# Kernel tuning notes

Hardware: AMD Instinct MI355X
Metric: run time of the kernel (lower is better)

The kernel has to match this reference:

```python
import jax, jax.numpy as jnp
import numpy as np

B, S, D, A, O = 4, 4096, 256, 64, 256

def setup_inputs() -> dict:
    key = jax.random.key(0)
    k1, k2, k3, k4, k5 = jax.random.split(key, 5)
    x = jax.random.normal(k1, (B, S, D), dtype=jnp.float32)
    # weights stored as [in, out] so projection is x @ W (same math as torch Linear W^T)
    Wk = jax.random.normal(k2, (D, A), dtype=jnp.float32) * (1.0 / np.sqrt(D))
    Wq = jax.random.normal(k3, (D, A), dtype=jnp.float32) * (1.0 / np.sqrt(D))
    Wv = jax.random.normal(k4, (D, A), dtype=jnp.float32) * (1.0 / np.sqrt(D))
    Wo = jax.random.normal(k5, (A, O), dtype=jnp.float32) * (1.0 / np.sqrt(A))
    return {"x": x, "Wk": Wk, "Wq": Wq, "Wv": Wv, "Wo": Wo}

def reference(x, Wk, Wq, Wv, Wo):
    # Single-head self-attention; dropout is identity at inference.
    k = x @ Wk  # [B,S,A]
    q = x @ Wq  # [B,S,A]
    v = x @ Wv  # [B,S,A]
    scale = 1.0 / jnp.sqrt(jnp.asarray(A, x.dtype))
    # logits[b,s,t] = k[b,s,:] . q[b,t,:]   (K @ Q^T in the torch code)
    logits = jnp.einsum('bsa,bta->bst', k, q) * scale
    w = jax.nn.softmax(logits, axis=-1)  # softmax over t
    # out[b,s,:] = sum_t w[b,s,t] * v[b,t,:]  (equivalent to V @ w^T then transpose)
    attn = jnp.einsum('bst,bta->bsa', w, v)
    return attn @ Wo  # [B,S,O]
```

## Files before the change

### kernel.cpp

```cpp
#include <hip/hip_runtime.h>


#define SQN 4096
#define AN 64
#define ON 256
#define QP 72

typedef short bf16x8 __attribute__((ext_vector_type(8)));
typedef float f32x4 __attribute__((ext_vector_type(4)));

__device__ __forceinline__ unsigned short f2bf(float f) {
    unsigned int u = __float_as_uint(f);
    u += 0x7fffu + ((u >> 16) & 1u);
    return (unsigned short)(u >> 16);
}
__device__ __forceinline__ unsigned int pack2(float a, float b) {
    return (unsigned int)f2bf(a) | ((unsigned int)f2bf(b) << 16);
}
__device__ __forceinline__ float exp2_hw(float x) {
    float r; asm("v_exp_f32 %0, %1" : "=v"(r) : "v"(x)); return r;
}

__global__ __launch_bounds__(256) void k_wtrans(
    const float* __restrict__ Wk, const float* __restrict__ Wq,
    const float* __restrict__ Wv, const float* __restrict__ Wo,
    unsigned short* __restrict__ WT, unsigned short* __restrict__ WoT)
{
    int bidx = blockIdx.x, tid = threadIdx.x;
    if (bidx < 24) {
        int m = bidx >> 3, chunk = bidx & 7;
        const float* src = (m == 0) ? Wk : (m == 1) ? Wq : Wv;
        float scl = (m == 1) ? 0.18033688011112042f : 1.0f;
        unsigned short* dst = WT + (m * 64 + chunk * 8) * 256;
        for (int idx = tid; idx < 8 * 256; idx += 256) {
            int a = chunk * 8 + (idx >> 8), d = idx & 255;
            dst[idx] = f2bf(src[d * 64 + a] * scl);
        }
    } else {
        int chunk = bidx - 24;
        for (int idx = tid; idx < 32 * 64; idx += 256) {
            int o = chunk * 32 + (idx >> 6), a = idx & 63;
            WoT[o * 64 + a] = f2bf(Wo[a * 256 + o]);
        }
    }
}

__global__ __launch_bounds__(256) void k_proj(
    const float* __restrict__ x, const unsigned short* __restrict__ WT,
    unsigned short* __restrict__ Ko, unsigned short* __restrict__ Qo,
    unsigned short* __restrict__ VTo)
{
    __shared__ unsigned short w_lds[192 * 128];
    __shared__ unsigned short x_lds[64 * 128];
    const int tid = threadIdx.x;
    const int wid = tid >> 6, lane = tid & 63, g = lane >> 4, li = lane & 15;
    const int s0 = blockIdx.x * 64;

    f32x4 acc[3][4] = {};
    for (int dh = 0; dh < 2; ++dh) {
        __syncthreads();
        {
            int row = tid >> 2, seg = tid & 3;
            const float4* src = (const float4*)(x + (size_t)(s0 + row) * 256 + dh * 128 + seg * 32);
            #pragma unroll
            for (int c = 0; c < 4; ++c) {
                float4 v0 = src[2 * c], v1 = src[2 * c + 1];
                uint4 o;
                o.x = pack2(v0.x, v0.y); o.y = pack2(v0.z, v0.w);
                o.z = pack2(v1.x, v1.y); o.w = pack2(v1.z, v1.w);
                *(uint4*)((char*)x_lds + row * 256 + ((seg * 64 + c * 16) ^ ((row & 7) << 4))) = o;
            }
        }
        {
            #pragma unroll
            for (int c = 0; c < 12; ++c) {
                int ch = tid + 256 * c;
                int row = ch >> 4, k16 = ch & 15;
                uint4 v = *(const uint4*)(WT + row * 256 + dh * 128 + k16 * 8);
                *(uint4*)((char*)w_lds + row * 256 + ((k16 * 16) ^ ((row & 7) << 4))) = v;
            }
        }
        __syncthreads();
        #pragma unroll
        for (int dc = 0; dc < 4; ++dc) {
            bf16x8 afr[4];
            #pragma unroll
            for (int sf = 0; sf < 4; ++sf) {
                int ar = sf * 16 + li;
                afr[sf] = *(const bf16x8*)((char*)x_lds + ar * 256 + ((dc * 64 + 16 * g) ^ ((ar & 7) << 4)));
            }
            #pragma unroll
            for (int c = 0; c < 3; ++c) {
                int br = (wid * 3 + c) * 16 + li;
                bf16x8 bfr = *(const bf16x8*)((char*)w_lds + br * 256 + ((dc * 64 + 16 * g) ^ ((br & 7) << 4)));
                #pragma unroll
                for (int sf = 0; sf < 4; ++sf)
                    acc[c][sf] = __builtin_amdgcn_mfma_f32_16x16x32_bf16(afr[sf], bfr, acc[c][sf], 0, 0, 0);
            }
        }
    }
    const int b = s0 >> 12;
    #pragma unroll
    for (int c = 0; c < 3; ++c) {
        int cfg = wid * 3 + c;
        int p = cfg >> 2, col = (cfg & 3) * 16 + li;
        if (p == 2) {
            int a = col;
            #pragma unroll
            for (int sf = 0; sf < 4; ++sf) {
                int sb = (s0 & 4095) + sf * 16 + 4 * g;
                uint2 u;
                u.x = pack2(acc[c][sf][0], acc[c][sf][1]);
                u.y = pack2(acc[c][sf][2], acc[c][sf][3]);
                *(uint2*)&VTo[(((size_t)(b * 64 + a)) << 12) + sb] = u;
            }
        } else {
            unsigned short* dst = (p == 0) ? Ko : Qo;
            #pragma unroll
            for (int sf = 0; sf < 4; ++sf)
                #pragma unroll
                for (int r = 0; r < 4; ++r)
                    dst[(size_t)(s0 + sf * 16 + 4 * g + r) * 64 + col] = f2bf(acc[c][sf][r]);
        }
    }
}

__global__ __launch_bounds__(256) void k_attn(
    const unsigned short* __restrict__ Qg, const unsigned short* __restrict__ Kg,
    const unsigned short* __restrict__ VTg,
    float* __restrict__ Opart, float* __restrict__ Mb, float* __restrict__ Lb)
{
    __shared__ unsigned short q_lds[2][64 * QP];
    __shared__ unsigned short v_lds[2][64 * QP];
    const int tid = threadIdx.x;
    const int wid = tid >> 6, lane = tid & 63, g = lane >> 4, li = lane & 15;
    const int b = blockIdx.x >> 8;
    const int s0 = ((blockIdx.x >> 2) & 63) * 64;
    const int h = blockIdx.x & 3;
    const int t_beg = h * 1024;
    const size_t base = (size_t)b * SQN * AN;
    const int srow = tid >> 2, sseg = tid & 3;

    bf16x8 kfrag[2];
    {
        const unsigned short* kp = Kg + base + (size_t)(s0 + wid * 16 + li) * 64;
        kfrag[0] = *(const bf16x8*)(kp + 8 * g);
        kfrag[1] = *(const bf16x8*)(kp + 32 + 8 * g);
    }

    {
        const uint4* qs = (const uint4*)(Qg + base + (size_t)(t_beg + srow) * 64 + sseg * 16);
        const uint4* vs = (const uint4*)(VTg + (((size_t)(b * 64 + srow)) << 12) + t_beg + sseg * 16);
        uint4 q0 = qs[0], q1 = qs[1], v0 = vs[0], v1 = vs[1];
        uint4* qd = (uint4*)&q_lds[0][srow * QP + sseg * 16];
        uint4* vd = (uint4*)&v_lds[0][srow * QP + sseg * 16];
        qd[0] = q0; qd[1] = q1; vd[0] = v0; vd[1] = v1;
    }
    __syncthreads();

    f32x4 ot[4] = {};
    float m_run = -1e30f, l_run = 0.0f;
    int cur = 0;

    for (int ti = 0; ti < 16; ++ti) {
        uint4 qr0, qr1, vr0, vr1;
        const bool pf = (ti < 15);
        if (pf) {
            int t1 = t_beg + (ti + 1) * 64;
            const uint4* qs = (const uint4*)(Qg + base + (size_t)(t1 + srow) * 64 + sseg * 16);
            const uint4* vs = (const uint4*)(VTg + (((size_t)(b * 64 + srow)) << 12) + t1 + sseg * 16);
            qr0 = qs[0]; qr1 = qs[1]; vr0 = vs[0]; vr1 = vs[1];
        }

        f32x4 st[4];
        #pragma unroll
        for (int tf = 0; tf < 4; ++tf) {
            f32x4 a0 = {};
            bf16x8 qa0 = *(const bf16x8*)&q_lds[cur][(tf * 16 + li) * QP + 8 * g];
            bf16x8 qa1 = *(const bf16x8*)&q_lds[cur][(tf * 16 + li) * QP + 32 + 8 * g];
            a0 = __builtin_amdgcn_mfma_f32_16x16x32_bf16(qa0, kfrag[0], a0, 0, 0, 0);
            a0 = __builtin_amdgcn_mfma_f32_16x16x32_bf16(qa1, kfrag[1], a0, 0, 0, 0);
            st[tf] = a0;
        }

        float tm = -1e30f;
        #pragma unroll
        for (int tf = 0; tf < 4; ++tf)
            #pragma unroll
            for (int r = 0; r < 4; ++r) tm = fmaxf(tm, st[tf][r]);
        tm = fmaxf(tm, __shfl_xor(tm, 16));
        tm = fmaxf(tm, __shfl_xor(tm, 32));
        float m_new = fmaxf(m_run, tm);
        float alpha = exp2_hw(m_run - m_new);
        float ts = 0.0f;
        unsigned int pk[4][2];
        #pragma unroll
        for (int tf = 0; tf < 4; ++tf) {
            float p0 = exp2_hw(st[tf][0] - m_new);
            float p1 = exp2_hw(st[tf][1] - m_new);
            float p2 = exp2_hw(st[tf][2] - m_new);
            float p3 = exp2_hw(st[tf][3] - m_new);
            ts += (p0 + p1) + (p2 + p3);
            pk[tf][0] = pack2(p0, p1);
            pk[tf][1] = pack2(p2, p3);
        }
        ts += __shfl_xor(ts, 16);
        ts += __shfl_xor(ts, 32);
        l_run = l_run * alpha + ts;
        m_run = m_new;
        #pragma unroll
        for (int af = 0; af < 4; ++af)
            #pragma unroll
            for (int r = 0; r < 4; ++r) ot[af][r] *= alpha;

        #pragma unroll
        for (int kc = 0; kc < 2; ++kc) {
            int s1 = ((2 * g) & 3) * 16 + li;
            int s2 = ((2 * g + 1) & 3) * 16 + li;
            unsigned int w0a = (unsigned)__shfl((int)pk[2 * kc][0], s1);
            unsigned int w1a = (unsigned)__shfl((int)pk[2 * kc][1], s1);
            unsigned int w2a = (unsigned)__shfl((int)pk[2 * kc][0], s2);
            unsigned int w3a = (unsigned)__shfl((int)pk[2 * kc][1], s2);
            unsigned int w0b = (unsigned)__shfl((int)pk[2 * kc + 1][0], s1);
            unsigned int w1b = (unsigned)__shfl((int)pk[2 * kc + 1][1], s1);
            unsigned int w2b = (unsigned)__shfl((int)pk[2 * kc + 1][0], s2);
            unsigned int w3b = (unsigned)__shfl((int)pk[2 * kc + 1][1], s2);
            union { unsigned int w[4]; bf16x8 v; } pb;
            bool hi = (g >= 2);
            pb.w[0] = hi ? w0b : w0a;
            pb.w[1] = hi ? w1b : w1a;
            pb.w[2] = hi ? w2b : w2a;
            pb.w[3] = hi ? w3b : w3a;
            #pragma unroll
            for (int af = 0; af < 4; ++af) {
                bf16x8 va = *(const bf16x8*)&v_lds[cur][(af * 16 + li) * QP + kc * 32 + 8 * g];
                ot[af] = __builtin_amdgcn_mfma_f32_16x16x32_bf16(va, pb.v, ot[af], 0, 0, 0);
            }
        }

        __syncthreads();
        if (pf) {
            uint4* qd = (uint4*)&q_lds[cur ^ 1][srow * QP + sseg * 16];
            uint4* vd = (uint4*)&v_lds[cur ^ 1][srow * QP + sseg * 16];
            qd[0] = qr0; qd[1] = qr1; vd[0] = vr0; vd[1] = vr1;
        }
        __syncthreads();
        cur ^= 1;
    }

    const int s = s0 + wid * 16 + li;
    float* op = Opart + ((size_t)((h * 4 + b) * 4096 + s)) * 64;
    #pragma unroll
    for (int af = 0; af < 4; ++af) {
        float4 o;
        o.x = ot[af][0]; o.y = ot[af][1]; o.z = ot[af][2]; o.w = ot[af][3];
        *(float4*)(op + af * 16 + 4 * g) = o;
    }
    if (g == 0) {
        Mb[(h * 4 + b) * 4096 + s] = m_run;
        Lb[(h * 4 + b) * 4096 + s] = l_run;
    }
}

__global__ __launch_bounds__(256) void k_combine_oproj(
    const float* __restrict__ Opart, const float* __restrict__ Mb, const float* __restrict__ Lb,
    const unsigned short* __restrict__ WoT, float* __restrict__ out)
{
    __shared__ unsigned short a_lds[64 * QP];
    const int tid = threadIdx.x;
    const int b = blockIdx.x >> 6;
    const int s0 = (blockIdx.x & 63) * 64;

    {
        int row = tid >> 2, seg = tid & 3;
        size_t ridx = (size_t)b * 4096 + s0 + row;
        float mm[4], ll[4];
        #pragma unroll
        for (int hh = 0; hh < 4; ++hh) { mm[hh] = Mb[hh * 16384 + ridx]; ll[hh] = Lb[hh * 16384 + ridx]; }
        float M = fmaxf(fmaxf(mm[0], mm[1]), fmaxf(mm[2], mm[3]));
        float w[4], denom = 0.0f;
        #pragma unroll
        for (int hh = 0; hh < 4; ++hh) { w[hh] = exp2_hw(mm[hh] - M); denom += w[hh] * ll[hh]; }
        float inv = 1.0f / denom;
        float av[16];
        #pragma unroll
        for (int j = 0; j < 16; ++j) av[j] = 0.0f;
        #pragma unroll
        for (int hh = 0; hh < 4; ++hh) {
            const float* op = Opart + ((size_t)hh * 16384 + ridx) * 64 + seg * 16;
            #pragma unroll
            for (int c = 0; c < 4; ++c) {
                float4 v = *(const float4*)(op + c * 4);
                av[4 * c + 0] += w[hh] * v.x; av[4 * c + 1] += w[hh] * v.y;
                av[4 * c + 2] += w[hh] * v.z; av[4 * c + 3] += w[hh] * v.w;
            }
        }
        uint4 u0, u1;
        u0.x = pack2(av[0] * inv, av[1] * inv);  u0.y = pack2(av[2] * inv, av[3] * inv);
        u0.z = pack2(av[4] * inv, av[5] * inv);  u0.w = pack2(av[6] * inv, av[7] * inv);
        u1.x = pack2(av[8] * inv, av[9] * inv);  u1.y = pack2(av[10] * inv, av[11] * inv);
        u1.z = pack2(av[12] * inv, av[13] * inv); u1.w = pack2(av[14] * inv, av[15] * inv);
        *(uint4*)&a_lds[row * QP + seg * 16] = u0;
        *(uint4*)&a_lds[row * QP + seg * 16 + 8] = u1;
    }
    __syncthreads();

    const int wid = tid >> 6, lane = tid & 63, g = lane >> 4, li = lane & 15;
    bf16x8 wf[4][2];
    #pragma unroll
    for (int of = 0; of < 4; ++of) {
        const unsigned short* wp = WoT + (size_t)(wid * 64 + of * 16 + li) * 64;
        wf[of][0] = *(const bf16x8*)(wp + 8 * g);
        wf[of][1] = *(const bf16x8*)(wp + 32 + 8 * g);
    }
    #pragma unroll
    for (int sf = 0; sf < 4; ++sf) {
        bf16x8 b0 = *(const bf16x8*)&a_lds[(sf * 16 + li) * QP + 8 * g];
        bf16x8 b1 = *(const bf16x8*)&a_lds[(sf * 16 + li) * QP + 32 + 8 * g];
        #pragma unroll
        for (int of = 0; of < 4; ++of) {
            f32x4 acc = {};
            acc = __builtin_amdgcn_mfma_f32_16x16x32_bf16(wf[of][0], b0, acc, 0, 0, 0);
            acc = __builtin_amdgcn_mfma_f32_16x16x32_bf16(wf[of][1], b1, acc, 0, 0, 0);
            float4 o;
            o.x = acc[0]; o.y = acc[1]; o.z = acc[2]; o.w = acc[3];
            *(float4*)&out[((size_t)b * 4096 + s0 + sf * 16 + li) * 256 + wid * 64 + of * 16 + 4 * g] = o;
        }
    }
}

extern "C" void kernel_launch(void* const* d_in, const int* in_sizes, int n_in,
                              void* d_out, int out_size, void* d_ws, size_t ws_size,
                              hipStream_t stream) {
    const float* x  = (const float*)d_in[0];
    const float* Wk = (const float*)d_in[1];
    const float* Wq = (const float*)d_in[2];
    const float* Wv = (const float*)d_in[3];
    const float* Wo = (const float*)d_in[4];
    float* out = (float*)d_out;

    char* ws = (char*)d_ws;
    unsigned short* WT  = (unsigned short*)(ws);
    unsigned short* WoT = (unsigned short*)(ws + 98304);
    unsigned short* Qb  = (unsigned short*)(ws + 131072);
    unsigned short* Kb  = (unsigned short*)(ws + 131072 + (1u<<21));
    unsigned short* VTb = (unsigned short*)(ws + 131072 + (2u<<21));
    float* Opart = (float*)(ws + 131072 + (3u<<21));
    float* Mb    = (float*)(ws + 131072 + (3u<<21) + (16u<<20));
    float* Lb    = (float*)(ws + 131072 + (3u<<21) + (17u<<20));

    k_wtrans<<<32, 256, 0, stream>>>(Wk, Wq, Wv, Wo, WT, WoT);
    k_proj<<<256, 256, 0, stream>>>(x, WT, Kb, Qb, VTb);
    k_attn<<<1024, 256, 0, stream>>>(Qb, Kb, VTb, Opart, Mb, Lb);
    k_combine_oproj<<<256, 256, 0, stream>>>(Opart, Mb, Lb, WoT, out);
}
```

Measured before the change: 135.0 us.

## Rework projection, attention and combine kernels with swizzled LDS and lazy rescaling

The projection kernel now handles 32 rows per block, reads weights directly from global memory instead of staging them in LDS, and launches twice as many blocks. The attention kernel swaps padded LDS rows for XOR-swizzled layouts, passes P through LDS instead of lane shuffles, and rescales the running max only when it grows past a threshold of 8. The combine kernel uses 16-row blocks to get more parallelism, and the bf16 conversion uses the hardware pack instruction. Together these aim to cut LDS bank conflicts, shuffle overhead and rescale work, but add more LDS traffic for P and rely on the threshold keeping exp values within range.

```diff
diff --git a/kernel.cpp b/kernel.cpp
--- a/kernel.cpp
+++ b/kernel.cpp
@@ -4,7 +4,6 @@
 #define SQN 4096
 #define AN 64
 #define ON 256
-#define QP 72
 
 typedef short bf16x8 __attribute__((ext_vector_type(8)));
 typedef float f32x4 __attribute__((ext_vector_type(4)));
@@ -14,8 +13,10 @@
     u += 0x7fffu + ((u >> 16) & 1u);
     return (unsigned short)(u >> 16);
 }
-__device__ __forceinline__ unsigned int pack2(float a, float b) {
-    return (unsigned int)f2bf(a) | ((unsigned int)f2bf(b) << 16);
+__device__ __forceinline__ unsigned int cvtpk(float lo, float hi) {
+    unsigned int r;
+    asm("v_cvt_pk_bf16_f32 %0, %1, %2" : "=v"(r) : "v"(lo), "v"(hi));
+    return r;
 }
 __device__ __forceinline__ float exp2_hw(float x) {
     float r; asm("v_exp_f32 %0, %1" : "=v"(r) : "v"(x)); return r;
@@ -50,74 +51,62 @@
     unsigned short* __restrict__ Ko, unsigned short* __restrict__ Qo,
     unsigned short* __restrict__ VTo)
 {
-    __shared__ unsigned short w_lds[192 * 128];
-    __shared__ unsigned short x_lds[64 * 128];
+    __shared__ unsigned short x_lds[32 * 256];
     const int tid = threadIdx.x;
     const int wid = tid >> 6, lane = tid & 63, g = lane >> 4, li = lane & 15;
-    const int s0 = blockIdx.x * 64;
-
-    f32x4 acc[3][4] = {};
-    for (int dh = 0; dh < 2; ++dh) {
-        __syncthreads();
-        {
-            int row = tid >> 2, seg = tid & 3;
-            const float4* src = (const float4*)(x + (size_t)(s0 + row) * 256 + dh * 128 + seg * 32);
-            #pragma unroll
-            for (int c = 0; c < 4; ++c) {
-                float4 v0 = src[2 * c], v1 = src[2 * c + 1];
-                uint4 o;
-                o.x = pack2(v0.x, v0.y); o.y = pack2(v0.z, v0.w);
-                o.z = pack2(v1.x, v1.y); o.w = pack2(v1.z, v1.w);
-                *(uint4*)((char*)x_lds + row * 256 + ((seg * 64 + c * 16) ^ ((row & 7) << 4))) = o;
-            }
-        }
-        {
-            #pragma unroll
-            for (int c = 0; c < 12; ++c) {
-                int ch = tid + 256 * c;
-                int row = ch >> 4, k16 = ch & 15;
-                uint4 v = *(const uint4*)(WT + row * 256 + dh * 128 + k16 * 8);
-                *(uint4*)((char*)w_lds + row * 256 + ((k16 * 16) ^ ((row & 7) << 4))) = v;
-            }
-        }
-        __syncthreads();
-        #pragma unroll
-        for (int dc = 0; dc < 4; ++dc) {
-            bf16x8 afr[4];
-            #pragma unroll
-            for (int sf = 0; sf < 4; ++sf) {
-                int ar = sf * 16 + li;
-                afr[sf] = *(const bf16x8*)((char*)x_lds + ar * 256 + ((dc * 64 + 16 * g) ^ ((ar & 7) << 4)));
-            }
-            #pragma unroll
-            for (int c = 0; c < 3; ++c) {
-                int br = (wid * 3 + c) * 16 + li;
-                bf16x8 bfr = *(const bf16x8*)((char*)w_lds + br * 256 + ((dc * 64 + 16 * g) ^ ((br & 7) << 4)));
-                #pragma unroll
-                for (int sf = 0; sf < 4; ++sf)
-                    acc[c][sf] = __builtin_amdgcn_mfma_f32_16x16x32_bf16(afr[sf], bfr, acc[c][sf], 0, 0, 0);
-            }
-        }
-    }
+    const int s0 = blockIdx.x * 32;
+
+    {
+        const float4* xs = (const float4*)(x + (size_t)s0 * 256);
+        #pragma unroll
+        for (int i = 0; i < 8; ++i) {
+            int idx4 = i * 256 + tid;
+            float4 v = xs[idx4];
+            int row = idx4 >> 6, q = idx4 & 63;
+            int unit = q >> 1, half = q & 1;
+            uint2 u; u.x = cvtpk(v.x, v.y); u.y = cvtpk(v.z, v.w);
+            *(uint2*)&x_lds[row * 256 + ((unit ^ (row & 7)) << 3) + half * 4] = u;
+        }
+    }
+    __syncthreads();
+
+    f32x4 acc[3][2] = {};
+    #pragma unroll
+    for (int dc = 0; dc < 8; ++dc) {
+        bf16x8 afr[2];
+        #pragma unroll
+        for (int sf = 0; sf < 2; ++sf) {
+            int ar = sf * 16 + li;
+            afr[sf] = *(const bf16x8*)&x_lds[ar * 256 + (((4 * dc + g) ^ (ar & 7)) << 3)];
+        }
+        #pragma unroll
+        for (int c = 0; c < 3; ++c) {
+            int wc = (wid * 3 + c) * 16 + li;
+            bf16x8 bfr = *(const bf16x8*)&WT[wc * 256 + dc * 32 + 8 * g];
+            #pragma unroll
+            for (int sf = 0; sf < 2; ++sf)
+                acc[c][sf] = __builtin_amdgcn_mfma_f32_16x16x32_bf16(afr[sf], bfr, acc[c][sf], 0, 0, 0);
+        }
+    }
+
     const int b = s0 >> 12;
     #pragma unroll
     for (int c = 0; c < 3; ++c) {
         int cfg = wid * 3 + c;
         int p = cfg >> 2, col = (cfg & 3) * 16 + li;
         if (p == 2) {
-            int a = col;
-            #pragma unroll
-            for (int sf = 0; sf < 4; ++sf) {
+            #pragma unroll
+            for (int sf = 0; sf < 2; ++sf) {
                 int sb = (s0 & 4095) + sf * 16 + 4 * g;
                 uint2 u;
-                u.x = pack2(acc[c][sf][0], acc[c][sf][1]);
-                u.y = pack2(acc[c][sf][2], acc[c][sf][3]);
-                *(uint2*)&VTo[(((size_t)(b * 64 + a)) << 12) + sb] = u;
+                u.x = cvtpk(acc[c][sf][0], acc[c][sf][1]);
+                u.y = cvtpk(acc[c][sf][2], acc[c][sf][3]);
+                *(uint2*)&VTo[(((size_t)(b * 64 + col)) << 12) + sb] = u;
             }
         } else {
             unsigned short* dst = (p == 0) ? Ko : Qo;
             #pragma unroll
-            for (int sf = 0; sf < 4; ++sf)
+            for (int sf = 0; sf < 2; ++sf)
                 #pragma unroll
                 for (int r = 0; r < 4; ++r)
                     dst[(size_t)(s0 + sf * 16 + 4 * g + r) * 64 + col] = f2bf(acc[c][sf][r]);
@@ -130,8 +119,9 @@
     const unsigned short* __restrict__ VTg,
     float* __restrict__ Opart, float* __restrict__ Mb, float* __restrict__ Lb)
 {
-    __shared__ unsigned short q_lds[2][64 * QP];
-    __shared__ unsigned short v_lds[2][64 * QP];
+    __shared__ unsigned short q_lds[2][64 * 64];
+    __shared__ unsigned short v_lds[2][64 * 64];
+    __shared__ unsigned int   p_lds[4][16 * 32];
     const int tid = threadIdx.x;
     const int wid = tid >> 6, lane = tid & 63, g = lane >> 4, li = lane & 15;
     const int b = blockIdx.x >> 8;
@@ -139,7 +129,8 @@
     const int h = blockIdx.x & 3;
     const int t_beg = h * 1024;
     const size_t base = (size_t)b * SQN * AN;
-    const int srow = tid >> 2, sseg = tid & 3;
+    const int srow = tid >> 2, sseg = tid & 3, r7 = srow & 7;
+    const int l7 = li & 7;
 
     bf16x8 kfrag[2];
     {
@@ -152,9 +143,10 @@
         const uint4* qs = (const uint4*)(Qg + base + (size_t)(t_beg + srow) * 64 + sseg * 16);
         const uint4* vs = (const uint4*)(VTg + (((size_t)(b * 64 + srow)) << 12) + t_beg + sseg * 16);
         uint4 q0 = qs[0], q1 = qs[1], v0 = vs[0], v1 = vs[1];
-        uint4* qd = (uint4*)&q_lds[0][srow * QP + sseg * 16];
-        uint4* vd = (uint4*)&v_lds[0][srow * QP + sseg * 16];
-        qd[0] = q0; qd[1] = q1; vd[0] = v0; vd[1] = v1;
+        *(uint4*)&q_lds[0][srow * 64 + (((2 * sseg) ^ r7) << 3)] = q0;
+        *(uint4*)&q_lds[0][srow * 64 + (((2 * sseg + 1) ^ r7) << 3)] = q1;
+        *(uint4*)&v_lds[0][srow * 64 + (((2 * sseg) ^ r7) << 3)] = v0;
+        *(uint4*)&v_lds[0][srow * 64 + (((2 * sseg + 1) ^ r7) << 3)] = v1;
     }
     __syncthreads();
 
@@ -176,8 +168,9 @@
         #pragma unroll
         for (int tf = 0; tf < 4; ++tf) {
             f32x4 a0 = {};
-            bf16x8 qa0 = *(const bf16x8*)&q_lds[cur][(tf * 16 + li) * QP + 8 * g];
-            bf16x8 qa1 = *(const bf16x8*)&q_lds[cur][(tf * 16 + li) * QP + 32 + 8 * g];
+            int qr = tf * 16 + li;
+            bf16x8 qa0 = *(const bf16x8*)&q_lds[cur][qr * 64 + ((g ^ l7) << 3)];
+            bf16x8 qa1 = *(const bf16x8*)&q_lds[cur][qr * 64 + (((4 + g) ^ l7) << 3)];
             a0 = __builtin_amdgcn_mfma_f32_16x16x32_bf16(qa0, kfrag[0], a0, 0, 0, 0);
             a0 = __builtin_amdgcn_mfma_f32_16x16x32_bf16(qa1, kfrag[1], a0, 0, 0, 0);
             st[tf] = a0;
@@ -190,59 +183,50 @@
             for (int r = 0; r < 4; ++r) tm = fmaxf(tm, st[tf][r]);
         tm = fmaxf(tm, __shfl_xor(tm, 16));
         tm = fmaxf(tm, __shfl_xor(tm, 32));
-        float m_new = fmaxf(m_run, tm);
-        float alpha = exp2_hw(m_run - m_new);
+        if (__any(tm > m_run + 8.0f)) {
+            float m_new = fmaxf(m_run, tm);
+            float alpha = exp2_hw(m_run - m_new);
+            #pragma unroll
+            for (int af = 0; af < 4; ++af)
+                #pragma unroll
+                for (int r = 0; r < 4; ++r) ot[af][r] *= alpha;
+            l_run *= alpha;
+            m_run = m_new;
+        }
         float ts = 0.0f;
-        unsigned int pk[4][2];
         #pragma unroll
         for (int tf = 0; tf < 4; ++tf) {
-            float p0 = exp2_hw(st[tf][0] - m_new);
-            float p1 = exp2_hw(st[tf][1] - m_new);
-            float p2 = exp2_hw(st[tf][2] - m_new);
-            float p3 = exp2_hw(st[tf][3] - m_new);
+            float p0 = exp2_hw(st[tf][0] - m_run);
+            float p1 = exp2_hw(st[tf][1] - m_run);
+            float p2 = exp2_hw(st[tf][2] - m_run);
+            float p3 = exp2_hw(st[tf][3] - m_run);
             ts += (p0 + p1) + (p2 + p3);
-            pk[tf][0] = pack2(p0, p1);
-            pk[tf][1] = pack2(p2, p3);
+            uint2 u; u.x = cvtpk(p0, p1); u.y = cvtpk(p2, p3);
+            int wi = 8 * tf + 2 * g;
+            *(uint2*)&p_lds[wid][li * 32 + (wi ^ (l7 << 2))] = u;
         }
         ts += __shfl_xor(ts, 16);
         ts += __shfl_xor(ts, 32);
-        l_run = l_run * alpha + ts;
-        m_run = m_new;
-        #pragma unroll
-        for (int af = 0; af < 4; ++af)
-            #pragma unroll
-            for (int r = 0; r < 4; ++r) ot[af][r] *= alpha;
+        l_run += ts;
 
         #pragma unroll
         for (int kc = 0; kc < 2; ++kc) {
-            int s1 = ((2 * g) & 3) * 16 + li;
-            int s2 = ((2 * g + 1) & 3) * 16 + li;
-            unsigned int w0a = (unsigned)__shfl((int)pk[2 * kc][0], s1);
-            unsigned int w1a = (unsigned)__shfl((int)pk[2 * kc][1], s1);
-            unsigned int w2a = (unsigned)__shfl((int)pk[2 * kc][0], s2);
-            unsigned int w3a = (unsigned)__shfl((int)pk[2 * kc][1], s2);
-            unsigned int w0b = (unsigned)__shfl((int)pk[2 * kc + 1][0], s1);
-            unsigned int w1b = (unsigned)__shfl((int)pk[2 * kc + 1][1], s1);
-            unsigned int w2b = (unsigned)__shfl((int)pk[2 * kc + 1][0], s2);
-            unsigned int w3b = (unsigned)__shfl((int)pk[2 * kc + 1][1], s2);
-            union { unsigned int w[4]; bf16x8 v; } pb;
-            bool hi = (g >= 2);
-            pb.w[0] = hi ? w0b : w0a;
-            pb.w[1] = hi ? w1b : w1a;
-            pb.w[2] = hi ? w2b : w2a;
-            pb.w[3] = hi ? w3b : w3a;
+            uint4 pw = *(const uint4*)&p_lds[wid][li * 32 + ((16 * kc + 4 * g) ^ (l7 << 2))];
+            union { uint4 u; bf16x8 v; } pb; pb.u = pw;
             #pragma unroll
             for (int af = 0; af < 4; ++af) {
-                bf16x8 va = *(const bf16x8*)&v_lds[cur][(af * 16 + li) * QP + kc * 32 + 8 * g];
+                int vr = af * 16 + li;
+                bf16x8 va = *(const bf16x8*)&v_lds[cur][vr * 64 + (((4 * kc + g) ^ (vr & 7)) << 3)];
                 ot[af] = __builtin_amdgcn_mfma_f32_16x16x32_bf16(va, pb.v, ot[af], 0, 0, 0);
             }
         }
 
         __syncthreads();
         if (pf) {
-            uint4* qd = (uint4*)&q_lds[cur ^ 1][srow * QP + sseg * 16];
-            uint4* vd = (uint4*)&v_lds[cur ^ 1][srow * QP + sseg * 16];
-            qd[0] = qr0; qd[1] = qr1; vd[0] = vr0; vd[1] = vr1;
+            *(uint4*)&q_lds[cur ^ 1][srow * 64 + (((2 * sseg) ^ r7) << 3)] = qr0;
+            *(uint4*)&q_lds[cur ^ 1][srow * 64 + (((2 * sseg + 1) ^ r7) << 3)] = qr1;
+            *(uint4*)&v_lds[cur ^ 1][srow * 64 + (((2 * sseg) ^ r7) << 3)] = vr0;
+            *(uint4*)&v_lds[cur ^ 1][srow * 64 + (((2 * sseg + 1) ^ r7) << 3)] = vr1;
         }
         __syncthreads();
         cur ^= 1;
@@ -266,13 +250,13 @@
     const float* __restrict__ Opart, const float* __restrict__ Mb, const float* __restrict__ Lb,
     const unsigned short* __restrict__ WoT, float* __restrict__ out)
 {
-    __shared__ unsigned short a_lds[64 * QP];
+    __shared__ unsigned short a_lds[16 * 64];
     const int tid = threadIdx.x;
-    const int b = blockIdx.x >> 6;
-    const int s0 = (blockIdx.x & 63) * 64;
+    const int b = blockIdx.x >> 8;
+    const int s0 = (blockIdx.x & 255) * 16;
 
     {
-        int row = tid >> 2, seg = tid & 3;
+        int row = tid >> 4, ac = (tid & 15) * 4;
         size_t ridx = (size_t)b * 4096 + s0 + row;
         float mm[4], ll[4];
         #pragma unroll
@@ -282,50 +266,32 @@
         #pragma unroll
         for (int hh = 0; hh < 4; ++hh) { w[hh] = exp2_hw(mm[hh] - M); denom += w[hh] * ll[hh]; }
         float inv = 1.0f / denom;
-        float av[16];
-        #pragma unroll
-        for (int j = 0; j < 16; ++j) av[j] = 0.0f;
+        float4 av = {0.f, 0.f, 0.f, 0.f};
         #pragma unroll
         for (int hh = 0; hh < 4; ++hh) {
-            const float* op = Opart + ((size_t)hh * 16384 + ridx) * 64 + seg * 16;
-            #pragma unroll
-            for (int c = 0; c < 4; ++c) {
-                float4 v = *(const float4*)(op + c * 4);
-                av[4 * c + 0] += w[hh] * v.x; av[4 * c + 1] += w[hh] * v.y;
-                av[4 * c + 2] += w[hh] * v.z; av[4 * c + 3] += w[hh] * v.w;
-            }
-        }
-        uint4 u0, u1;
-        u0.x = pack2(av[0] * inv, av[1] * inv);  u0.y = pack2(av[2] * inv, av[3] * inv);
-        u0.z = pack2(av[4] * inv, av[5] * inv);  u0.w = pack2(av[6] * inv, av[7] * inv);
-        u1.x = pack2(av[8] * inv, av[9] * inv);  u1.y = pack2(av[10] * inv, av[11] * inv);
-        u1.z = pack2(av[12] * inv, av[13] * inv); u1.w = pack2(av[14] * inv, av[15] * inv);
-        *(uint4*)&a_lds[row * QP + seg * 16] = u0;
-        *(uint4*)&a_lds[row * QP + seg * 16 + 8] = u1;
+            float4 v = *(const float4*)&Opart[((size_t)hh * 16384 + ridx) * 64 + ac];
+            av.x += w[hh] * v.x; av.y += w[hh] * v.y; av.z += w[hh] * v.z; av.w += w[hh] * v.w;
+        }
+        int unit = ac >> 3;
+        uint2 u; u.x = cvtpk(av.x * inv, av.y * inv); u.y = cvtpk(av.z * inv, av.w * inv);
+        *(uint2*)&a_lds[row * 64 + ((unit ^ (row & 7)) << 3) + (ac & 7)] = u;
     }
     __syncthreads();
 
     const int wid = tid >> 6, lane = tid & 63, g = lane >> 4, li = lane & 15;
-    bf16x8 wf[4][2];
+    bf16x8 b0 = *(const bf16x8*)&a_lds[li * 64 + ((g ^ (li & 7)) << 3)];
+    bf16x8 b1 = *(const bf16x8*)&a_lds[li * 64 + (((4 + g) ^ (li & 7)) << 3)];
     #pragma unroll
     for (int of = 0; of < 4; ++of) {
         const unsigned short* wp = WoT + (size_t)(wid * 64 + of * 16 + li) * 64;
-        wf[of][0] = *(const bf16x8*)(wp + 8 * g);
-        wf[of][1] = *(const bf16x8*)(wp + 32 + 8 * g);
-    }
-    #pragma unroll
-    for (int sf = 0; sf < 4; ++sf) {
-        bf16x8 b0 = *(const bf16x8*)&a_lds[(sf * 16 + li) * QP + 8 * g];
-        bf16x8 b1 = *(const bf16x8*)&a_lds[(sf * 16 + li) * QP + 32 + 8 * g];
-        #pragma unroll
-        for (int of = 0; of < 4; ++of) {
-            f32x4 acc = {};
-            acc = __builtin_amdgcn_mfma_f32_16x16x32_bf16(wf[of][0], b0, acc, 0, 0, 0);
-            acc = __builtin_amdgcn_mfma_f32_16x16x32_bf16(wf[of][1], b1, acc, 0, 0, 0);
-            float4 o;
-            o.x = acc[0]; o.y = acc[1]; o.z = acc[2]; o.w = acc[3];
-            *(float4*)&out[((size_t)b * 4096 + s0 + sf * 16 + li) * 256 + wid * 64 + of * 16 + 4 * g] = o;
-        }
+        bf16x8 w0 = *(const bf16x8*)(wp + 8 * g);
+        bf16x8 w1 = *(const bf16x8*)(wp + 32 + 8 * g);
+        f32x4 acc = {};
+        acc = __builtin_amdgcn_mfma_f32_16x16x32_bf16(w0, b0, acc, 0, 0, 0);
+        acc = __builtin_amdgcn_mfma_f32_16x16x32_bf16(w1, b1, acc, 0, 0, 0);
+        float4 o;
+        o.x = acc[0]; o.y = acc[1]; o.z = acc[2]; o.w = acc[3];
+        *(float4*)&out[((size_t)b * 4096 + s0 + li) * 256 + wid * 64 + of * 16 + 4 * g] = o;
     }
 }
 
@@ -350,7 +316,7 @@
     float* Lb    = (float*)(ws + 131072 + (3u<<21) + (17u<<20));
 
     k_wtrans<<<32, 256, 0, stream>>>(Wk, Wq, Wv, Wo, WT, WoT);
-    k_proj<<<256, 256, 0, stream>>>(x, WT, Kb, Qb, VTb);
+    k_proj<<<512, 256, 0, stream>>>(x, WT, Kb, Qb, VTb);
     k_attn<<<1024, 256, 0, stream>>>(Qb, Kb, VTb, Opart, Mb, Lb);
-    k_combine_oproj<<<256, 256, 0, stream>>>(Opart, Mb, Lb, WoT, out);
-}
+    k_combine_oproj<<<1024, 256, 0, stream>>>(Opart, Mb, Lb, WoT, out);
+}
```

Result: faster. 126.7 us (-6.1%).
